# Kernel tuning notes

Measured on AMD Instinct MI355X. Metric: run time of the kernel, lower is better.

Reference implementation:

```python
import jax, jax.numpy as jnp
import numpy as np

D = 4096          # input_dims
P = 1             # p in Get_Atten_map_mc
NUM_IMG = 16
N_PER = 64        # objects per image
R_PER = 512       # relations per image
LN_EPS = 1e-5


def _linear_params(key, out_dim, in_dim):
    kw, kb = jax.random.split(key)
    w = jax.random.normal(kw, (out_dim, in_dim), jnp.float32) * 0.02
    b = jax.random.normal(kb, (out_dim,), jnp.float32) * 0.02
    return w, b


def setup_inputs() -> dict:
    key = jax.random.key(0)
    ks = jax.random.split(key, 12)
    N = NUM_IMG * N_PER
    R = NUM_IMG * R_PER

    obj_feats = jax.random.normal(ks[0], (N, D), jnp.float32)
    phr_feats = jax.random.normal(ks[1], (R, D), jnp.float32)

    # im_inds: uniform N_PER objects per image
    im_inds = jnp.repeat(jnp.arange(NUM_IMG, dtype=jnp.int64), N_PER)

    # rel_inds: [img_idx, subj_global, obj_global], R_PER rels per image,
    # subject/object indices local-to-image then offset to global ids.
    subj_loc = jax.random.randint(ks[2], (NUM_IMG, R_PER), 0, N_PER)
    obj_loc = jax.random.randint(ks[3], (NUM_IMG, R_PER), 0, N_PER)
    offs = (jnp.arange(NUM_IMG) * N_PER)[:, None]
    img_col = jnp.repeat(jnp.arange(NUM_IMG), R_PER)
    rel_inds = jnp.stack(
        [img_col, (subj_loc + offs).reshape(-1), (obj_loc + offs).reshape(-1)], axis=1
    ).astype(jnp.int64)

    Ws_w, Ws_b = _linear_params(ks[4], D, D)       # ws
    Wo_w, Wo_b = _linear_params(ks[5], D, D)       # wo
    Ww_w, Ww_b = _linear_params(ks[6], P, D)       # w (attention logits)
    Wc_w, Wc_b = _linear_params(ks[7], D // 2, D)  # conv Linear
    Wt1_w, Wt1_b = _linear_params(ks[8], D // 4, D)
    Wt2_w, Wt2_b = _linear_params(ks[9], D, D // 4)
    ln_g = jnp.ones((D // 4,), jnp.float32)
    ln_b = jnp.zeros((D // 4,), jnp.float32)

    return {
        "obj_feats": obj_feats, "phr_feats": phr_feats,
        "im_inds": im_inds, "rel_inds": rel_inds, "num_img": NUM_IMG,
        "Ws_w": Ws_w, "Ws_b": Ws_b, "Wo_w": Wo_w, "Wo_b": Wo_b,
        "Ww_w": Ww_w, "Ww_b": Ww_b, "Wc_w": Wc_w, "Wc_b": Wc_b,
        "Wt1_w": Wt1_w, "Wt1_b": Wt1_b, "ln_g": ln_g, "ln_b": ln_b,
        "Wt2_w": Wt2_w, "Wt2_b": Wt2_b,
    }


def reference(obj_feats, phr_feats, im_inds, rel_inds, num_img,
              Ws_w, Ws_b, Wo_w, Wo_b, Ww_w, Ww_b, Wc_w, Wc_b,
              Wt1_w, Wt1_b, ln_g, ln_b, Wt2_w, Wt2_b):
    N, d = obj_feats.shape
    n_per = N // num_img
    R = rel_inds.shape[0]
    r_per = R // num_img
    p = Ww_w.shape[0]

    # ws/wo projections over all objects (original recomputes them per image
    # on the full obj_feats -- identical math, computed once here).
    ws_all = obj_feats @ Ws_w.T + Ws_b
    wo_all = obj_feats @ Wo_w.T + Wo_b

    subj = rel_inds[:, 1]
    objc = rel_inds[:, 2]
    prod = ws_all[subj] * wo_all[objc]               # [R, D]
    atten_f = (prod * phr_feats) @ Ww_w.T + Ww_b     # [R, p]

    # conv on object features
    conv_all = jax.nn.relu(obj_feats @ Wc_w.T + Wc_b)  # [N, D/2]

    subj_i = subj.reshape(num_img, r_per)
    objc_i = objc.reshape(num_img, r_per)
    af_i = atten_f.reshape(num_img, r_per, p)
    conv_i = conv_all.reshape(num_img, n_per, -1)

    self_mask = 1.0 - jnp.eye(n_per, dtype=jnp.float32)[:, :, None]  # [n,n,1]

    def per_image(s, o, af, conv_feats):
        head = jnp.minimum(s.min(), o.min())
        A = jnp.zeros((n_per, n_per, p), jnp.float32).at[s - head, o - head].add(af)
        A = jax.nn.sigmoid(A) * self_mask
        A = A / A.sum(1)                               # [n,n,p] / [n,p] (col-normalize)
        A2 = jnp.concatenate([A, A.transpose(1, 0, 2)], axis=-1)  # [n,n,2p]
        # mc_matmul: concat of per-channel mm -> channel-major reshape
        return jnp.einsum('ijc,jd->icd', A2, conv_feats).reshape(n_per, -1)

    ctx = jax.vmap(per_image)(subj_i, objc_i, af_i, conv_i)  # [num_img, n, 2p*D/2]
    ctx = ctx.reshape(N, -1)                                  # [N, D]

    # trans: Linear -> LayerNorm -> ReLU -> Linear
    h = ctx @ Wt1_w.T + Wt1_b
    mu = h.mean(-1, keepdims=True)
    var = ((h - mu) ** 2).mean(-1, keepdims=True)
    h = (h - mu) * jax.lax.rsqrt(var + LN_EPS) * ln_g + ln_b
    h = jax.nn.relu(h)
    out = h @ Wt2_w.T + Wt2_b

    return jax.nn.relu(obj_feats + out)
```

## Files before the change

### kernel.cpp

```cpp
#include <hip/hip_runtime.h>
#include <hip/hip_bf16.h>
#include <math.h>

#define D_   4096
#define NIMG 16
#define NPER 64
#define RPER 512
#define NTOT 1024
#define RTOT 8192
#define DC   2048
#define DT   1024
#define LDO  10240

typedef __attribute__((ext_vector_type(4))) float f32x4;
typedef __attribute__((ext_vector_type(8))) short bf16x8;

#define GLD16(gp, lp) __builtin_amdgcn_global_load_lds( \
    (const __attribute__((address_space(1))) unsigned int*)(gp), \
    (__attribute__((address_space(3))) unsigned int*)(lp), 16, 0, 0)

struct Cast4 {
    const float* src0; const float* src1; const float* src2; const float* src3;
    __hip_bfloat16* dst0; __hip_bfloat16* dst1; __hip_bfloat16* dst2; __hip_bfloat16* dst3;
    int s1, s2, s3;
};

__global__ __launch_bounds__(256) void cast_multi(Cast4 a)
{
    const int b = blockIdx.x;
    const float* s; __hip_bfloat16* d; int rb;
    if (b < a.s1)      { s = a.src0; d = a.dst0; rb = b; }
    else if (b < a.s2) { s = a.src1; d = a.dst1; rb = b - a.s1; }
    else if (b < a.s3) { s = a.src2; d = a.dst2; rb = b - a.s2; }
    else               { s = a.src3; d = a.dst3; rb = b - a.s3; }
    const int i = (rb * 256 + threadIdx.x) * 8;
    float4 v0 = *(const float4*)(s + i);
    float4 v1 = *(const float4*)(s + i + 4);
    union { __hip_bfloat16 h[8]; ushort4 u[2]; } cv;
    cv.h[0] = __float2bfloat16(v0.x); cv.h[1] = __float2bfloat16(v0.y);
    cv.h[2] = __float2bfloat16(v0.z); cv.h[3] = __float2bfloat16(v0.w);
    cv.h[4] = __float2bfloat16(v1.x); cv.h[5] = __float2bfloat16(v1.y);
    cv.h[6] = __float2bfloat16(v1.z); cv.h[7] = __float2bfloat16(v1.w);
    *(ushort4*)(d + i)     = cv.u[0];
    *(ushort4*)(d + i + 4) = cv.u[1];
}

__global__ __launch_bounds__(256) void concat_bias(
    const float* __restrict__ b0, const float* __restrict__ b1,
    const float* __restrict__ b2, float* __restrict__ cb)
{
    const int i = blockIdx.x * 256 + threadIdx.x;
    float v;
    if (i < 4096) v = b0[i];
    else if (i < 8192) v = b1[i - 4096];
    else v = b2[i - 8192];
    cb[i] = v;
}

template<int BM, int BN>
__global__ __launch_bounds__(256) void gemm_p2(
    const ushort* __restrict__ A, const ushort* __restrict__ B,
    const float* __restrict__ bias, const float* __restrict__ resid,
    float* __restrict__ C, int M, int K, int ldc, int mode, int reluStart)
{
    constexpr int MREP = BM / 32;
    constexpr int NREP = BN / 32;
    constexpr int SLOTS = (BM + BN) * 4;
    constexpr int NPW = SLOTS / 256;
    constexpr int BUFE = SLOTS * 8;

    __shared__ ushort lds[3][BUFE];

    const int t = threadIdx.x;
    const int lane = t & 63;
    const int wid = t >> 6;
    const int wr = wid >> 1, wc = wid & 1;

    const int MT = M / BM;
    const int G = gridDim.x;
    const int bid = blockIdx.x;
    const int wgid = (bid & 7) * (G >> 3) + (bid >> 3);
    const int nt = wgid / MT, mt = wgid % MT;
    const int bm = mt * BM, bn = nt * BN;

    const ushort* gp[NPW];
    int loff[NPW];
#pragma unroll
    for (int i = 0; i < NPW; ++i) {
        const int slot = i * 256 + t;
        const bool isA = slot < BM * 4;
        const int s2 = isA ? slot : slot - BM * 4;
        const int row = s2 >> 2;
        const int q = (s2 & 3) ^ (row & 3);
        gp[i] = (isA ? A + (size_t)(bm + row) * K : B + (size_t)(bn + row) * K) + q * 8;
        loff[i] = slot * 8;
    }

    auto stage = [&](int b, int kpos) {
#pragma unroll
        for (int i = 0; i < NPW; ++i) GLD16(gp[i] + kpos, &lds[b][loff[i]]);
    };

    int aoff[MREP], boff[NREP];
    const int sx = (((lane >> 4) ^ (lane & 3))) << 3;
#pragma unroll
    for (int m = 0; m < MREP; ++m)
        aoff[m] = (wr * (BM / 2) + (lane & 15) + m * 16) * 32 + sx;
#pragma unroll
    for (int n = 0; n < NREP; ++n)
        boff[n] = BM * 32 + (wc * (BN / 2) + (lane & 15) + n * 16) * 32 + sx;

    f32x4 acc[MREP][NREP] = {};

    const int NT = K >> 5;
    stage(0, 0);
    stage(1, 32);
    if constexpr (NPW == 2) asm volatile("s_waitcnt vmcnt(2)" ::: "memory");
    else if constexpr (NPW == 3) asm volatile("s_waitcnt vmcnt(3)" ::: "memory");
    else asm volatile("s_waitcnt vmcnt(4)" ::: "memory");
    __builtin_amdgcn_sched_barrier(0);
    __builtin_amdgcn_s_barrier();
    __builtin_amdgcn_sched_barrier(0);

    for (int tt = 0; tt < NT; ++tt) {
        const bool pf = (tt + 2 < NT);
        if (pf) stage((tt + 2) % 3, (tt + 2) << 5);
        __builtin_amdgcn_sched_barrier(0);

        const ushort* lb = lds[tt % 3];
        bf16x8 af[MREP], bfv[NREP];
#pragma unroll
        for (int m = 0; m < MREP; ++m) af[m] = *(const bf16x8*)(lb + aoff[m]);
#pragma unroll
        for (int n = 0; n < NREP; ++n) bfv[n] = *(const bf16x8*)(lb + boff[n]);
#pragma unroll
        for (int m = 0; m < MREP; ++m)
#pragma unroll
            for (int n = 0; n < NREP; ++n)
                acc[m][n] = __builtin_amdgcn_mfma_f32_16x16x32_bf16(
                    af[m], bfv[n], acc[m][n], 0, 0, 0);

        __builtin_amdgcn_sched_barrier(0);
        if (pf) {
            if constexpr (NPW == 2) asm volatile("s_waitcnt vmcnt(2)" ::: "memory");
            else if constexpr (NPW == 3) asm volatile("s_waitcnt vmcnt(3)" ::: "memory");
            else asm volatile("s_waitcnt vmcnt(4)" ::: "memory");
        } else {
            asm volatile("s_waitcnt vmcnt(0)" ::: "memory");
        }
        __builtin_amdgcn_sched_barrier(0);
        __builtin_amdgcn_s_barrier();
        __builtin_amdgcn_sched_barrier(0);
    }

    const int col0 = bn + wc * (BN / 2) + (lane & 15);
    const int row0 = bm + wr * (BM / 2) + ((lane >> 4) << 2);
#pragma unroll
    for (int m = 0; m < MREP; ++m) {
#pragma unroll
        for (int n = 0; n < NREP; ++n) {
            const int cn = col0 + n * 16;
            const float bz = bias[cn];
#pragma unroll
            for (int rg = 0; rg < 4; ++rg) {
                const int gm = row0 + m * 16 + rg;
                float v = acc[m][n][rg] + bz;
                if (mode == 2) v = fmaxf(v + resid[(size_t)gm * ldc + cn], 0.f);
                else if (mode == 3 && cn >= reluStart) v = fmaxf(v, 0.f);
                C[(size_t)gm * ldc + cn] = v;
            }
        }
    }
}

__global__ __launch_bounds__(256) void atten_kernel(
    const float* __restrict__ allout, const float* __restrict__ phr,
    const int* __restrict__ rel, const float* __restrict__ Www,
    const float* __restrict__ Wwb, float* __restrict__ atten)
{
    const int r = blockIdx.x;
    const int s = rel[r * 3 + 1], o = rel[r * 3 + 2];
    const int t = threadIdx.x;
    const float4* pws = (const float4*)(allout + (size_t)s * LDO);
    const float4* pwo = (const float4*)(allout + (size_t)o * LDO + 4096);
    const float4* pph = (const float4*)(phr + (size_t)r * D_);
    const float4* pww = (const float4*)Www;
    float sum = 0.f;
    for (int qq = t; qq < D_ / 4; qq += 256) {
        float4 a = pws[qq], b = pwo[qq], c = pph[qq], w = pww[qq];
        sum += a.x * b.x * c.x * w.x + a.y * b.y * c.y * w.y
             + a.z * b.z * c.z * w.z + a.w * b.w * c.w * w.w;
    }
    for (int off = 32; off > 0; off >>= 1) sum += __shfl_down(sum, off);
    __shared__ float red[4];
    if ((t & 63) == 0) red[t >> 6] = sum;
    __syncthreads();
    if (t == 0) atten[r] = red[0] + red[1] + red[2] + red[3] + Wwb[0];
}

__global__ __launch_bounds__(256) void build_A(
    const int* __restrict__ rel, const float* __restrict__ atten,
    float* __restrict__ Anorm)
{
    const int g = blockIdx.x;
    const int t = threadIdx.x;
    __shared__ float Am[64][64];
    __shared__ float S[64];
    __shared__ int headSh;
    for (int i = t; i < 4096; i += 256) ((float*)Am)[i] = 0.f;
    if (t == 0) headSh = 0x7fffffff;

    int lmin = 0x7fffffff;
    for (int rr = t; rr < RPER; rr += 256) {
        const int base = (g * RPER + rr) * 3;
        lmin = min(lmin, min(rel[base + 1], rel[base + 2]));
    }
    for (int off = 32; off > 0; off >>= 1) lmin = min(lmin, __shfl_down(lmin, off));
    __syncthreads();
    if ((t & 63) == 0) atomicMin(&headSh, lmin);
    __syncthreads();
    const int head = headSh;

    for (int rr = t; rr < RPER; rr += 256) {
        const int base = (g * RPER + rr) * 3;
        atomicAdd(&Am[rel[base + 1] - head][rel[base + 2] - head],
                  atten[g * RPER + rr]);
    }
    __syncthreads();

    for (int idx = t; idx < 4096; idx += 256) {
        const int i = idx >> 6, j = idx & 63;
        float v = 1.f / (1.f + expf(-Am[i][j]));
        if (i == j) v = 0.f;
        Am[i][j] = v;
    }
    __syncthreads();

    if (t < 64) {
        float sum = 0.f;
        for (int k = 0; k < 64; ++k) sum += Am[t][k];
        S[t] = sum;
    }
    __syncthreads();

    float* outg = Anorm + (size_t)g * 4096;
    for (int idx = t; idx < 4096; idx += 256) {
        const int j = idx & 63;
        outg[idx] = ((const float*)Am)[idx] / S[j];
    }
}

__device__ __forceinline__ void fma4(float4& d, float s, const float4 c) {
    d.x = fmaf(s, c.x, d.x); d.y = fmaf(s, c.y, d.y);
    d.z = fmaf(s, c.z, d.z); d.w = fmaf(s, c.w, d.w);
}
__device__ __forceinline__ void st4bf(__hip_bfloat16* p, float4 v) {
    union { __hip_bfloat16 h[4]; ushort4 u; } cv;
    cv.h[0] = __float2bfloat16(v.x); cv.h[1] = __float2bfloat16(v.y);
    cv.h[2] = __float2bfloat16(v.z); cv.h[3] = __float2bfloat16(v.w);
    *(ushort4*)p = cv.u;
}

__global__ __launch_bounds__(256) void ctx_kernel(
    const float* __restrict__ Anorm, const float* __restrict__ allout,
    __hip_bfloat16* __restrict__ ctx)
{
    const int g = blockIdx.x >> 6;
    const int i = blockIdx.x & 63;
    const int t = threadIdx.x;
    __shared__ float Arow[64], Acol[64];
    if (t < 64) Arow[t] = Anorm[(size_t)g * 4096 + i * 64 + t];
    else if (t < 128) { const int j = t - 64; Acol[j] = Anorm[(size_t)g * 4096 + j * 64 + i]; }
    __syncthreads();

    const float* cg = allout + (size_t)g * NPER * LDO + 8192;
    float4 a0 = {0,0,0,0}, a1 = a0, a2 = a0, a3 = a0;
    for (int j = 0; j < 64; ++j) {
        const float ar = Arow[j], ac = Acol[j];
        float4 c0 = *(const float4*)(cg + (size_t)j * LDO + (t << 2));
        float4 c1 = *(const float4*)(cg + (size_t)j * LDO + 1024 + (t << 2));
        fma4(a0, ar, c0); fma4(a1, ar, c1);
        fma4(a2, ac, c0); fma4(a3, ac, c1);
    }
    __hip_bfloat16* crow = ctx + (size_t)(g * NPER + i) * D_;
    st4bf(crow + (t << 2),        a0);
    st4bf(crow + 1024 + (t << 2), a1);
    st4bf(crow + 2048 + (t << 2), a2);
    st4bf(crow + 3072 + (t << 2), a3);
}

__global__ __launch_bounds__(256) void ln_relu_kernel(
    const float* __restrict__ h, const float* __restrict__ gamma,
    const float* __restrict__ beta, __hip_bfloat16* __restrict__ hb)
{
    const int row = blockIdx.x;
    const int t = threadIdx.x;
    const float* hr = h + (size_t)row * DT;
    float4 v = *(const float4*)(hr + (t << 2));
    float s  = v.x + v.y + v.z + v.w;
    float ss = v.x * v.x + v.y * v.y + v.z * v.z + v.w * v.w;
    for (int off = 32; off > 0; off >>= 1) {
        s  += __shfl_down(s, off);
        ss += __shfl_down(ss, off);
    }
    __shared__ float rs[4], rss[4];
    if ((t & 63) == 0) { rs[t >> 6] = s; rss[t >> 6] = ss; }
    __syncthreads();
    const float tot  = rs[0] + rs[1] + rs[2] + rs[3];
    const float tot2 = rss[0] + rss[1] + rss[2] + rss[3];
    const float mu   = tot * (1.f / DT);
    const float var  = tot2 * (1.f / DT) - mu * mu;
    const float rstd = rsqrtf(var + 1e-5f);
    float4 g4 = *(const float4*)(gamma + (t << 2));
    float4 b4 = *(const float4*)(beta + (t << 2));
    float4 o;
    o.x = fmaxf(fmaf((v.x - mu) * rstd, g4.x, b4.x), 0.f);
    o.y = fmaxf(fmaf((v.y - mu) * rstd, g4.y, b4.y), 0.f);
    o.z = fmaxf(fmaf((v.z - mu) * rstd, g4.z, b4.z), 0.f);
    o.w = fmaxf(fmaf((v.w - mu) * rstd, g4.w, b4.w), 0.f);
    st4bf(hb + (size_t)row * DT + (t << 2), o);
}

extern "C" void kernel_launch(void* const* d_in, const int* in_sizes, int n_in,
                              void* d_out, int out_size, void* d_ws, size_t ws_size,
                              hipStream_t stream)
{
    const float* obj   = (const float*)d_in[0];
    const float* phr   = (const float*)d_in[1];
    const int*   rel   = (const int*)d_in[3];
    const float* Ws_w  = (const float*)d_in[5];
    const float* Ws_b  = (const float*)d_in[6];
    const float* Wo_w  = (const float*)d_in[7];
    const float* Wo_b  = (const float*)d_in[8];
    const float* Ww_w  = (const float*)d_in[9];
    const float* Ww_b  = (const float*)d_in[10];
    const float* Wc_w  = (const float*)d_in[11];
    const float* Wc_b  = (const float*)d_in[12];
    const float* Wt1_w = (const float*)d_in[13];
    const float* Wt1_b = (const float*)d_in[14];
    const float* ln_g  = (const float*)d_in[15];
    const float* ln_b  = (const float*)d_in[16];
    const float* Wt2_w = (const float*)d_in[17];
    const float* Wt2_b = (const float*)d_in[18];
    float* out = (float*)d_out;

    float* ws = (float*)d_ws;
    __hip_bfloat16* wbuf   = (__hip_bfloat16*)ws;
    __hip_bfloat16* wbuf_t1 = wbuf;
    __hip_bfloat16* wbuf_t2 = wbuf + 4194304;
    __hip_bfloat16* obj_bf = (__hip_bfloat16*)(ws + 20971520);
    __hip_bfloat16* ctx_bf = obj_bf;
    float* allout = ws + 23068672;
    float* h_f32  = allout;
    __hip_bfloat16* h_bf = (__hip_bfloat16*)(allout + 1048576);
    float* atten  = ws + 33554432;
    float* Anorm  = ws + 33562624;
    float* cbias  = ws + 33628160;

    const dim3 blk(256);

    Cast4 c1;
    c1.src0 = obj;  c1.dst0 = obj_bf;
    c1.src1 = Ws_w; c1.dst1 = wbuf;
    c1.src2 = Wo_w; c1.dst2 = wbuf + 16777216;
    c1.src3 = Wc_w; c1.dst3 = wbuf + 33554432;
    c1.s1 = 2048; c1.s2 = 10240; c1.s3 = 18432;
    cast_multi<<<dim3(22528), blk, 0, stream>>>(c1);

    concat_bias<<<dim3(40), blk, 0, stream>>>(Ws_b, Wo_b, Wc_b, cbias);

    gemm_p2<128, 128><<<dim3(640), blk, 0, stream>>>(
        (const ushort*)obj_bf, (const ushort*)wbuf, cbias, nullptr,
        allout, NTOT, D_, LDO, 3, 8192);

    Cast4 c2;
    c2.src0 = Wt1_w; c2.dst0 = wbuf_t1;
    c2.src1 = Wt2_w; c2.dst1 = wbuf_t2;
    c2.src2 = Wt1_w; c2.dst2 = wbuf_t1;
    c2.src3 = Wt1_w; c2.dst3 = wbuf_t1;
    c2.s1 = 2048; c2.s2 = 1 << 30; c2.s3 = 1 << 30;
    cast_multi<<<dim3(4096), blk, 0, stream>>>(c2);

    atten_kernel<<<dim3(RTOT), blk, 0, stream>>>(allout, phr, rel, Ww_w, Ww_b, atten);
    build_A<<<dim3(NIMG), blk, 0, stream>>>(rel, atten, Anorm);
    ctx_kernel<<<dim3(1024), blk, 0, stream>>>(Anorm, allout, ctx_bf);

    gemm_p2<64, 64><<<dim3(256), blk, 0, stream>>>(
        (const ushort*)ctx_bf, (const ushort*)wbuf_t1, Wt1_b, nullptr,
        h_f32, NTOT, D_, DT, 0, 0);
    ln_relu_kernel<<<dim3(NTOT), blk, 0, stream>>>(h_f32, ln_g, ln_b, h_bf);
    gemm_p2<128, 128><<<dim3(256), blk, 0, stream>>>(
        (const ushort*)h_bf, (const ushort*)wbuf_t2, Wt2_b, obj,
        out, NTOT, DT, D_, 2, 0);
}
```

Baseline: 326.7 us.

## Fuse fp32-to-bf16 weight conversion into GEMM B-operand loading

Removes the separate cast kernels that converted all weight matrices (about 40M fp32 elements) to bf16 in workspace. The GEMMs now read fp32 weights directly into registers, convert them, and write bf16 into LDS, while the activation operand keeps the async global-to-LDS path. The object cast and bias concatenation are merged into one launch. This avoids a large write-then-read round trip, but the GEMMs now load twice the weight bytes and spend VALU and register time converting inside the main loop.

```diff
diff --git a/kernel.cpp b/kernel.cpp
--- a/kernel.cpp
+++ b/kernel.cpp
@@ -19,55 +19,53 @@
     (const __attribute__((address_space(1))) unsigned int*)(gp), \
     (__attribute__((address_space(3))) unsigned int*)(lp), 16, 0, 0)
 
-struct Cast4 {
-    const float* src0; const float* src1; const float* src2; const float* src3;
-    __hip_bfloat16* dst0; __hip_bfloat16* dst1; __hip_bfloat16* dst2; __hip_bfloat16* dst3;
-    int s1, s2, s3;
-};
-
-__global__ __launch_bounds__(256) void cast_multi(Cast4 a)
-{
-    const int b = blockIdx.x;
-    const float* s; __hip_bfloat16* d; int rb;
-    if (b < a.s1)      { s = a.src0; d = a.dst0; rb = b; }
-    else if (b < a.s2) { s = a.src1; d = a.dst1; rb = b - a.s1; }
-    else if (b < a.s3) { s = a.src2; d = a.dst2; rb = b - a.s2; }
-    else               { s = a.src3; d = a.dst3; rb = b - a.s3; }
-    const int i = (rb * 256 + threadIdx.x) * 8;
-    float4 v0 = *(const float4*)(s + i);
-    float4 v1 = *(const float4*)(s + i + 4);
-    union { __hip_bfloat16 h[8]; ushort4 u[2]; } cv;
-    cv.h[0] = __float2bfloat16(v0.x); cv.h[1] = __float2bfloat16(v0.y);
-    cv.h[2] = __float2bfloat16(v0.z); cv.h[3] = __float2bfloat16(v0.w);
-    cv.h[4] = __float2bfloat16(v1.x); cv.h[5] = __float2bfloat16(v1.y);
-    cv.h[6] = __float2bfloat16(v1.z); cv.h[7] = __float2bfloat16(v1.w);
-    *(ushort4*)(d + i)     = cv.u[0];
-    *(ushort4*)(d + i + 4) = cv.u[1];
-}
-
-__global__ __launch_bounds__(256) void concat_bias(
+template<int N> __device__ __forceinline__ void waitvm() {
+    asm volatile("s_waitcnt vmcnt(%0)" :: "n"(N) : "memory");
+}
+
+__global__ __launch_bounds__(256) void cast_obj_bias(
+    const float* __restrict__ obj, __hip_bfloat16* __restrict__ obj_bf,
     const float* __restrict__ b0, const float* __restrict__ b1,
     const float* __restrict__ b2, float* __restrict__ cb)
 {
-    const int i = blockIdx.x * 256 + threadIdx.x;
-    float v;
-    if (i < 4096) v = b0[i];
-    else if (i < 8192) v = b1[i - 4096];
-    else v = b2[i - 8192];
-    cb[i] = v;
+    const int b = blockIdx.x;
+    if (b < 2048) {
+        const int i = (b * 256 + threadIdx.x) * 8;
+        float4 v0 = *(const float4*)(obj + i);
+        float4 v1 = *(const float4*)(obj + i + 4);
+        union { __hip_bfloat16 h[8]; ushort4 u[2]; } cv;
+        cv.h[0] = __float2bfloat16(v0.x); cv.h[1] = __float2bfloat16(v0.y);
+        cv.h[2] = __float2bfloat16(v0.z); cv.h[3] = __float2bfloat16(v0.w);
+        cv.h[4] = __float2bfloat16(v1.x); cv.h[5] = __float2bfloat16(v1.y);
+        cv.h[6] = __float2bfloat16(v1.z); cv.h[7] = __float2bfloat16(v1.w);
+        *(ushort4*)(obj_bf + i)     = cv.u[0];
+        *(ushort4*)(obj_bf + i + 4) = cv.u[1];
+    } else {
+        const int i = (b - 2048) * 256 + threadIdx.x;
+        float v;
+        if (i < 4096) v = b0[i];
+        else if (i < 8192) v = b1[i - 4096];
+        else v = b2[i - 8192];
+        cb[i] = v;
+    }
 }
 
 template<int BM, int BN>
-__global__ __launch_bounds__(256) void gemm_p2(
-    const ushort* __restrict__ A, const ushort* __restrict__ B,
+__global__ __launch_bounds__(256) void gemm_h(
+    const ushort* __restrict__ A,
+    const float* __restrict__ B0, const float* __restrict__ B1,
+    const float* __restrict__ B2, int ns1, int ns2,
     const float* __restrict__ bias, const float* __restrict__ resid,
     float* __restrict__ C, int M, int K, int ldc, int mode, int reluStart)
 {
     constexpr int MREP = BM / 32;
     constexpr int NREP = BN / 32;
-    constexpr int SLOTS = (BM + BN) * 4;
-    constexpr int NPW = SLOTS / 256;
-    constexpr int BUFE = SLOTS * 8;
+    constexpr int SA = BM * 4;
+    constexpr int SB = BN * 4;
+    constexpr int NA = SA / 256;
+    constexpr int NB = SB / 256;
+    constexpr int INFLIGHT = NA + 2 * NB;
+    constexpr int BUFE = (SA + SB) * 8;
 
     __shared__ ushort lds[3][BUFE];
 
@@ -83,22 +81,53 @@
     const int nt = wgid / MT, mt = wgid % MT;
     const int bm = mt * BM, bn = nt * BN;
 
-    const ushort* gp[NPW];
-    int loff[NPW];
-#pragma unroll
-    for (int i = 0; i < NPW; ++i) {
+    const ushort* gpa[NA];
+    int lofa[NA];
+#pragma unroll
+    for (int i = 0; i < NA; ++i) {
         const int slot = i * 256 + t;
-        const bool isA = slot < BM * 4;
-        const int s2 = isA ? slot : slot - BM * 4;
-        const int row = s2 >> 2;
-        const int q = (s2 & 3) ^ (row & 3);
-        gp[i] = (isA ? A + (size_t)(bm + row) * K : B + (size_t)(bn + row) * K) + q * 8;
-        loff[i] = slot * 8;
-    }
-
-    auto stage = [&](int b, int kpos) {
-#pragma unroll
-        for (int i = 0; i < NPW; ++i) GLD16(gp[i] + kpos, &lds[b][loff[i]]);
+        const int row = slot >> 2;
+        const int q = (slot & 3) ^ (row & 3);
+        gpa[i] = A + (size_t)(bm + row) * K + q * 8;
+        lofa[i] = slot * 8;
+    }
+    const float* gpb[NB];
+    int lofb[NB];
+#pragma unroll
+    for (int i = 0; i < NB; ++i) {
+        const int sb = i * 256 + t;
+        const int row = sb >> 2;
+        const int q = (sb & 3) ^ (row & 3);
+        const int gn = bn + row;
+        const float* bp = (gn < ns1) ? B0 + (size_t)gn * K
+                        : (gn < ns2) ? B1 + (size_t)(gn - ns1) * K
+                                     : B2 + (size_t)(gn - ns2) * K;
+        gpb[i] = bp + q * 8;
+        lofb[i] = (SA + sb) * 8;
+    }
+
+    auto stageA = [&](int b, int kpos) {
+#pragma unroll
+        for (int i = 0; i < NA; ++i) GLD16(gpa[i] + kpos, &lds[b][lofa[i]]);
+    };
+    auto loadB = [&](f32x4 (&br)[NB][2], int kpos) {
+#pragma unroll
+        for (int i = 0; i < NB; ++i) {
+            br[i][0] = *(const f32x4*)(gpb[i] + kpos);
+            br[i][1] = *(const f32x4*)(gpb[i] + kpos + 4);
+        }
+    };
+    auto writeB = [&](f32x4 (&br)[NB][2], int b) {
+#pragma unroll
+        for (int i = 0; i < NB; ++i) {
+            union { __hip_bfloat16 h[8]; uint4 q; } cv;
+#pragma unroll
+            for (int j = 0; j < 4; ++j) {
+                cv.h[j]     = __float2bfloat16(br[i][0][j]);
+                cv.h[4 + j] = __float2bfloat16(br[i][1][j]);
+            }
+            *(uint4*)&lds[b][lofb[i]] = cv.q;
+        }
     };
 
     int aoff[MREP], boff[NREP];
@@ -108,23 +137,28 @@
         aoff[m] = (wr * (BM / 2) + (lane & 15) + m * 16) * 32 + sx;
 #pragma unroll
     for (int n = 0; n < NREP; ++n)
-        boff[n] = BM * 32 + (wc * (BN / 2) + (lane & 15) + n * 16) * 32 + sx;
+        boff[n] = SA * 8 + (wc * (BN / 2) + (lane & 15) + n * 16) * 32 + sx;
 
     f32x4 acc[MREP][NREP] = {};
+    f32x4 br0[NB][2], br1[NB][2];
 
     const int NT = K >> 5;
-    stage(0, 0);
-    stage(1, 32);
-    if constexpr (NPW == 2) asm volatile("s_waitcnt vmcnt(2)" ::: "memory");
-    else if constexpr (NPW == 3) asm volatile("s_waitcnt vmcnt(3)" ::: "memory");
-    else asm volatile("s_waitcnt vmcnt(4)" ::: "memory");
+
+    stageA(0, 0);  loadB(br0, 0);
+    stageA(1, 32); loadB(br1, 32);
+    waitvm<INFLIGHT>();
+    writeB(br0, 0);
+    asm volatile("s_waitcnt lgkmcnt(0)" ::: "memory");
     __builtin_amdgcn_sched_barrier(0);
     __builtin_amdgcn_s_barrier();
     __builtin_amdgcn_sched_barrier(0);
 
-    for (int tt = 0; tt < NT; ++tt) {
-        const bool pf = (tt + 2 < NT);
-        if (pf) stage((tt + 2) % 3, (tt + 2) << 5);
+    auto step = [&](int tt, auto& brW, auto& brL) {
+        const bool more = (tt + 2 < NT);
+        if (more) {
+            stageA((tt + 2) % 3, (tt + 2) << 5);
+            loadB(brL, (tt + 2) << 5);
+        }
         __builtin_amdgcn_sched_barrier(0);
 
         const ushort* lb = lds[tt % 3];
@@ -139,18 +173,22 @@
             for (int n = 0; n < NREP; ++n)
                 acc[m][n] = __builtin_amdgcn_mfma_f32_16x16x32_bf16(
                     af[m], bfv[n], acc[m][n], 0, 0, 0);
-
         __builtin_amdgcn_sched_barrier(0);
-        if (pf) {
-            if constexpr (NPW == 2) asm volatile("s_waitcnt vmcnt(2)" ::: "memory");
-            else if constexpr (NPW == 3) asm volatile("s_waitcnt vmcnt(3)" ::: "memory");
-            else asm volatile("s_waitcnt vmcnt(4)" ::: "memory");
-        } else {
-            asm volatile("s_waitcnt vmcnt(0)" ::: "memory");
+
+        if (tt + 1 < NT) {
+            if (more) waitvm<INFLIGHT>(); else waitvm<0>();
+            __builtin_amdgcn_sched_barrier(0);
+            writeB(brW, (tt + 1) % 3);
+            asm volatile("s_waitcnt lgkmcnt(0)" ::: "memory");
+            __builtin_amdgcn_sched_barrier(0);
+            __builtin_amdgcn_s_barrier();
+            __builtin_amdgcn_sched_barrier(0);
         }
-        __builtin_amdgcn_sched_barrier(0);
-        __builtin_amdgcn_s_barrier();
-        __builtin_amdgcn_sched_barrier(0);
+    };
+
+    for (int tt = 0; tt < NT; tt += 2) {
+        step(tt,     br1, br0);
+        step(tt + 1, br0, br1);
     }
 
     const int col0 = bn + wc * (BN / 2) + (lane & 15);
@@ -345,51 +383,33 @@
     float* out = (float*)d_out;
 
     float* ws = (float*)d_ws;
-    __hip_bfloat16* wbuf   = (__hip_bfloat16*)ws;
-    __hip_bfloat16* wbuf_t1 = wbuf;
-    __hip_bfloat16* wbuf_t2 = wbuf + 4194304;
-    __hip_bfloat16* obj_bf = (__hip_bfloat16*)(ws + 20971520);
+    __hip_bfloat16* obj_bf = (__hip_bfloat16*)ws;
     __hip_bfloat16* ctx_bf = obj_bf;
-    float* allout = ws + 23068672;
+    float* allout = ws + 2097152;
     float* h_f32  = allout;
     __hip_bfloat16* h_bf = (__hip_bfloat16*)(allout + 1048576);
-    float* atten  = ws + 33554432;
-    float* Anorm  = ws + 33562624;
-    float* cbias  = ws + 33628160;
+    float* atten  = ws + 12582912;
+    float* Anorm  = ws + 12591104;
+    float* cbias  = ws + 12656640;
 
     const dim3 blk(256);
-
-    Cast4 c1;
-    c1.src0 = obj;  c1.dst0 = obj_bf;
-    c1.src1 = Ws_w; c1.dst1 = wbuf;
-    c1.src2 = Wo_w; c1.dst2 = wbuf + 16777216;
-    c1.src3 = Wc_w; c1.dst3 = wbuf + 33554432;
-    c1.s1 = 2048; c1.s2 = 10240; c1.s3 = 18432;
-    cast_multi<<<dim3(22528), blk, 0, stream>>>(c1);
-
-    concat_bias<<<dim3(40), blk, 0, stream>>>(Ws_b, Wo_b, Wc_b, cbias);
-
-    gemm_p2<128, 128><<<dim3(640), blk, 0, stream>>>(
-        (const ushort*)obj_bf, (const ushort*)wbuf, cbias, nullptr,
-        allout, NTOT, D_, LDO, 3, 8192);
-
-    Cast4 c2;
-    c2.src0 = Wt1_w; c2.dst0 = wbuf_t1;
-    c2.src1 = Wt2_w; c2.dst1 = wbuf_t2;
-    c2.src2 = Wt1_w; c2.dst2 = wbuf_t1;
-    c2.src3 = Wt1_w; c2.dst3 = wbuf_t1;
-    c2.s1 = 2048; c2.s2 = 1 << 30; c2.s3 = 1 << 30;
-    cast_multi<<<dim3(4096), blk, 0, stream>>>(c2);
+    const int BIG = 1 << 30;
+
+    cast_obj_bias<<<dim3(2088), blk, 0, stream>>>(obj, obj_bf, Ws_b, Wo_b, Wc_b, cbias);
+
+    gemm_h<128, 128><<<dim3(640), blk, 0, stream>>>(
+        (const ushort*)obj_bf, Ws_w, Wo_w, Wc_w, 4096, 8192,
+        cbias, nullptr, allout, NTOT, D_, LDO, 3, 8192);
 
     atten_kernel<<<dim3(RTOT), blk, 0, stream>>>(allout, phr, rel, Ww_w, Ww_b, atten);
     build_A<<<dim3(NIMG), blk, 0, stream>>>(rel, atten, Anorm);
     ctx_kernel<<<dim3(1024), blk, 0, stream>>>(Anorm, allout, ctx_bf);
 
-    gemm_p2<64, 64><<<dim3(256), blk, 0, stream>>>(
-        (const ushort*)ctx_bf, (const ushort*)wbuf_t1, Wt1_b, nullptr,
-        h_f32, NTOT, D_, DT, 0, 0);
+    gemm_h<64, 64><<<dim3(256), blk, 0, stream>>>(
+        (const ushort*)ctx_bf, Wt1_w, Wt1_w, Wt1_w, BIG, BIG,
+        Wt1_b, nullptr, h_f32, NTOT, D_, DT, 0, 0);
     ln_relu_kernel<<<dim3(NTOT), blk, 0, stream>>>(h_f32, ln_g, ln_b, h_bf);
-    gemm_p2<128, 128><<<dim3(256), blk, 0, stream>>>(
-        (const ushort*)h_bf, (const ushort*)wbuf_t2, Wt2_b, obj,
-        out, NTOT, DT, D_, 2, 0);
-}
+    gemm_h<128, 128><<<dim3(256), blk, 0, stream>>>(
+        (const ushort*)h_bf, Wt2_w, Wt2_w, Wt2_w, BIG, BIG,
+        Wt2_b, obj, out, NTOT, DT, D_, 2, 0);
+}
```

Result: slower. 494.1 us (+51.2%).

## Reassociate attention mixing after Wt1 projection and fuse mixing with LayerNorm

Applied to the files above, without the earlier changes.

The code now computes the first trans projection on the conv features (conv @ Wt1 split into subject and object halves) before applying the per-image attention matrix, rather than building the 4096-wide context and multiplying it by Wt1. The Wt1 weight is rearranged during casting so a single GEMM with K=2048 produces both halves, and the A-mixing, bias add, LayerNorm and ReLU are fused into one kernel. The first GEMM writes the conv output straight to bf16 with ReLU, and the row stride shrinks to 8192. Casting and bias concatenation are merged into one launch, and the LDS swizzle pattern is changed. This removes the ctx buffer, the wide K=4096 GEMM and a separate LN pass, at the cost of a different rounding order.

```diff
diff --git a/kernel.cpp b/kernel.cpp
--- a/kernel.cpp
+++ b/kernel.cpp
@@ -10,7 +10,7 @@
 #define RTOT 8192
 #define DC   2048
 #define DT   1024
-#define LDO  10240
+#define LDA  8192
 
 typedef __attribute__((ext_vector_type(4))) float f32x4;
 typedef __attribute__((ext_vector_type(8))) short bf16x8;
@@ -19,49 +19,88 @@
     (const __attribute__((address_space(1))) unsigned int*)(gp), \
     (__attribute__((address_space(3))) unsigned int*)(lp), 16, 0, 0)
 
-struct Cast4 {
-    const float* src0; const float* src1; const float* src2; const float* src3;
-    __hip_bfloat16* dst0; __hip_bfloat16* dst1; __hip_bfloat16* dst2; __hip_bfloat16* dst3;
-    int s1, s2, s3;
-};
-
-__global__ __launch_bounds__(256) void cast_multi(Cast4 a)
+template<int N> __device__ __forceinline__ void waitvm() {
+    asm volatile("s_waitcnt vmcnt(%0)" :: "n"(N) : "memory");
+}
+
+__device__ __forceinline__ void fma4(float4& d, float s, const float4 c) {
+    d.x = fmaf(s, c.x, d.x); d.y = fmaf(s, c.y, d.y);
+    d.z = fmaf(s, c.z, d.z); d.w = fmaf(s, c.w, d.w);
+}
+__device__ __forceinline__ void st4bf(__hip_bfloat16* p, float4 v) {
+    union { __hip_bfloat16 h[4]; ushort4 u; } cv;
+    cv.h[0] = __float2bfloat16(v.x); cv.h[1] = __float2bfloat16(v.y);
+    cv.h[2] = __float2bfloat16(v.z); cv.h[3] = __float2bfloat16(v.w);
+    *(ushort4*)p = cv.u;
+}
+
+__global__ __launch_bounds__(256) void cast_all(
+    const float* __restrict__ obj, __hip_bfloat16* __restrict__ obj_bf,
+    const float* __restrict__ Ws, const float* __restrict__ Wo,
+    const float* __restrict__ Wc, __hip_bfloat16* __restrict__ wbuf,
+    const float* __restrict__ b0, const float* __restrict__ b1,
+    const float* __restrict__ b2, float* __restrict__ cb)
 {
     const int b = blockIdx.x;
-    const float* s; __hip_bfloat16* d; int rb;
-    if (b < a.s1)      { s = a.src0; d = a.dst0; rb = b; }
-    else if (b < a.s2) { s = a.src1; d = a.dst1; rb = b - a.s1; }
-    else if (b < a.s3) { s = a.src2; d = a.dst2; rb = b - a.s2; }
-    else               { s = a.src3; d = a.dst3; rb = b - a.s3; }
-    const int i = (rb * 256 + threadIdx.x) * 8;
-    float4 v0 = *(const float4*)(s + i);
-    float4 v1 = *(const float4*)(s + i + 4);
+    if (b < 22528) {
+        const float* s; __hip_bfloat16* d; int rb;
+        if (b < 2048)       { s = obj; d = obj_bf;          rb = b; }
+        else if (b < 10240) { s = Ws;  d = wbuf;            rb = b - 2048; }
+        else if (b < 18432) { s = Wo;  d = wbuf + 16777216; rb = b - 10240; }
+        else                { s = Wc;  d = wbuf + 33554432; rb = b - 18432; }
+        const int i = (rb * 256 + threadIdx.x) * 8;
+        float4 v0 = *(const float4*)(s + i);
+        float4 v1 = *(const float4*)(s + i + 4);
+        union { __hip_bfloat16 h[8]; ushort4 u[2]; } cv;
+        cv.h[0] = __float2bfloat16(v0.x); cv.h[1] = __float2bfloat16(v0.y);
+        cv.h[2] = __float2bfloat16(v0.z); cv.h[3] = __float2bfloat16(v0.w);
+        cv.h[4] = __float2bfloat16(v1.x); cv.h[5] = __float2bfloat16(v1.y);
+        cv.h[6] = __float2bfloat16(v1.z); cv.h[7] = __float2bfloat16(v1.w);
+        *(ushort4*)(d + i)     = cv.u[0];
+        *(ushort4*)(d + i + 4) = cv.u[1];
+    } else {
+        const int i = (b - 22528) * 256 + threadIdx.x;
+        float v;
+        if (i < 4096) v = b0[i];
+        else if (i < 8192) v = b1[i - 4096];
+        else v = b2[i - 8192];
+        cb[i] = v;
+    }
+}
+
+__global__ __launch_bounds__(256) void cast2(
+    const float* __restrict__ Wt1, const float* __restrict__ Wt2,
+    __hip_bfloat16* __restrict__ wt1r, __hip_bfloat16* __restrict__ wt2b)
+{
+    const int b = blockIdx.x;
+    const int t = threadIdx.x;
+    const float* s; __hip_bfloat16* d;
+    if (b < 2048) {
+        const int r = b, c = t * 8;
+        s = Wt1 + (size_t)(r & 1023) * 4096 + (r >> 10) * 2048 + c;
+        d = wt1r + (size_t)r * 2048 + c;
+    } else {
+        const int i = ((b - 2048) * 256 + t) * 8;
+        s = Wt2 + i;
+        d = wt2b + i;
+    }
+    float4 v0 = *(const float4*)s;
+    float4 v1 = *(const float4*)(s + 4);
     union { __hip_bfloat16 h[8]; ushort4 u[2]; } cv;
     cv.h[0] = __float2bfloat16(v0.x); cv.h[1] = __float2bfloat16(v0.y);
     cv.h[2] = __float2bfloat16(v0.z); cv.h[3] = __float2bfloat16(v0.w);
     cv.h[4] = __float2bfloat16(v1.x); cv.h[5] = __float2bfloat16(v1.y);
     cv.h[6] = __float2bfloat16(v1.z); cv.h[7] = __float2bfloat16(v1.w);
-    *(ushort4*)(d + i)     = cv.u[0];
-    *(ushort4*)(d + i + 4) = cv.u[1];
-}
-
-__global__ __launch_bounds__(256) void concat_bias(
-    const float* __restrict__ b0, const float* __restrict__ b1,
-    const float* __restrict__ b2, float* __restrict__ cb)
-{
-    const int i = blockIdx.x * 256 + threadIdx.x;
-    float v;
-    if (i < 4096) v = b0[i];
-    else if (i < 8192) v = b1[i - 4096];
-    else v = b2[i - 8192];
-    cb[i] = v;
+    *(ushort4*)d       = cv.u[0];
+    *(ushort4*)(d + 4) = cv.u[1];
 }
 
 template<int BM, int BN>
 __global__ __launch_bounds__(256) void gemm_p2(
     const ushort* __restrict__ A, const ushort* __restrict__ B,
     const float* __restrict__ bias, const float* __restrict__ resid,
-    float* __restrict__ C, int M, int K, int ldc, int mode, int reluStart)
+    float* __restrict__ C, __hip_bfloat16* __restrict__ C2,
+    int M, int K, int ldc, int mode, int reluStart)
 {
     constexpr int MREP = BM / 32;
     constexpr int NREP = BN / 32;
@@ -91,7 +130,7 @@
         const bool isA = slot < BM * 4;
         const int s2 = isA ? slot : slot - BM * 4;
         const int row = s2 >> 2;
-        const int q = (s2 & 3) ^ (row & 3);
+        const int q = (s2 & 3) ^ ((row >> 1) & 3);
         gp[i] = (isA ? A + (size_t)(bm + row) * K : B + (size_t)(bn + row) * K) + q * 8;
         loff[i] = slot * 8;
     }
@@ -102,7 +141,7 @@
     };
 
     int aoff[MREP], boff[NREP];
-    const int sx = (((lane >> 4) ^ (lane & 3))) << 3;
+    const int sx = (((lane >> 4) ^ ((lane >> 1) & 3))) << 3;
 #pragma unroll
     for (int m = 0; m < MREP; ++m)
         aoff[m] = (wr * (BM / 2) + (lane & 15) + m * 16) * 32 + sx;
@@ -115,9 +154,9 @@
     const int NT = K >> 5;
     stage(0, 0);
     stage(1, 32);
-    if constexpr (NPW == 2) asm volatile("s_waitcnt vmcnt(2)" ::: "memory");
-    else if constexpr (NPW == 3) asm volatile("s_waitcnt vmcnt(3)" ::: "memory");
-    else asm volatile("s_waitcnt vmcnt(4)" ::: "memory");
+    if constexpr (NPW == 2) waitvm<2>();
+    else if constexpr (NPW == 3) waitvm<3>();
+    else waitvm<4>();
     __builtin_amdgcn_sched_barrier(0);
     __builtin_amdgcn_s_barrier();
     __builtin_amdgcn_sched_barrier(0);
@@ -142,11 +181,11 @@
 
         __builtin_amdgcn_sched_barrier(0);
         if (pf) {
-            if constexpr (NPW == 2) asm volatile("s_waitcnt vmcnt(2)" ::: "memory");
-            else if constexpr (NPW == 3) asm volatile("s_waitcnt vmcnt(3)" ::: "memory");
-            else asm volatile("s_waitcnt vmcnt(4)" ::: "memory");
+            if constexpr (NPW == 2) waitvm<2>();
+            else if constexpr (NPW == 3) waitvm<3>();
+            else waitvm<4>();
         } else {
-            asm volatile("s_waitcnt vmcnt(0)" ::: "memory");
+            waitvm<0>();
         }
         __builtin_amdgcn_sched_barrier(0);
         __builtin_amdgcn_s_barrier();
@@ -160,14 +199,24 @@
 #pragma unroll
         for (int n = 0; n < NREP; ++n) {
             const int cn = col0 + n * 16;
-            const float bz = bias[cn];
+            const float bz = bias ? bias[cn] : 0.f;
 #pragma unroll
             for (int rg = 0; rg < 4; ++rg) {
                 const int gm = row0 + m * 16 + rg;
                 float v = acc[m][n][rg] + bz;
-                if (mode == 2) v = fmaxf(v + resid[(size_t)gm * ldc + cn], 0.f);
-                else if (mode == 3 && cn >= reluStart) v = fmaxf(v, 0.f);
-                C[(size_t)gm * ldc + cn] = v;
+                if (mode == 2) {
+                    v = fmaxf(v + resid[(size_t)gm * ldc + cn], 0.f);
+                    C[(size_t)gm * ldc + cn] = v;
+                } else if (mode == 4) {
+                    if (cn < reluStart) {
+                        C[(size_t)gm * ldc + cn] = v;
+                    } else {
+                        C2[(size_t)gm * 2048 + (cn - 8192)] =
+                            __float2bfloat16(fmaxf(v, 0.f));
+                    }
+                } else {
+                    C[(size_t)gm * ldc + cn] = v;
+                }
             }
         }
     }
@@ -181,8 +230,8 @@
     const int r = blockIdx.x;
     const int s = rel[r * 3 + 1], o = rel[r * 3 + 2];
     const int t = threadIdx.x;
-    const float4* pws = (const float4*)(allout + (size_t)s * LDO);
-    const float4* pwo = (const float4*)(allout + (size_t)o * LDO + 4096);
+    const float4* pws = (const float4*)(allout + (size_t)s * LDA);
+    const float4* pwo = (const float4*)(allout + (size_t)o * LDA + 4096);
     const float4* pph = (const float4*)(phr + (size_t)r * D_);
     const float4* pww = (const float4*)Www;
     float sum = 0.f;
@@ -250,53 +299,30 @@
     }
 }
 
-__device__ __forceinline__ void fma4(float4& d, float s, const float4 c) {
-    d.x = fmaf(s, c.x, d.x); d.y = fmaf(s, c.y, d.y);
-    d.z = fmaf(s, c.z, d.z); d.w = fmaf(s, c.w, d.w);
-}
-__device__ __forceinline__ void st4bf(__hip_bfloat16* p, float4 v) {
-    union { __hip_bfloat16 h[4]; ushort4 u; } cv;
-    cv.h[0] = __float2bfloat16(v.x); cv.h[1] = __float2bfloat16(v.y);
-    cv.h[2] = __float2bfloat16(v.z); cv.h[3] = __float2bfloat16(v.w);
-    *(ushort4*)p = cv.u;
-}
-
-__global__ __launch_bounds__(256) void ctx_kernel(
-    const float* __restrict__ Anorm, const float* __restrict__ allout,
-    __hip_bfloat16* __restrict__ ctx)
+__global__ __launch_bounds__(256) void amult_ln(
+    const float* __restrict__ Anorm, const float* __restrict__ P,
+    const float* __restrict__ w1b, const float* __restrict__ gamma,
+    const float* __restrict__ beta, __hip_bfloat16* __restrict__ hb)
 {
     const int g = blockIdx.x >> 6;
     const int i = blockIdx.x & 63;
     const int t = threadIdx.x;
-    __shared__ float Arow[64], Acol[64];
-    if (t < 64) Arow[t] = Anorm[(size_t)g * 4096 + i * 64 + t];
-    else if (t < 128) { const int j = t - 64; Acol[j] = Anorm[(size_t)g * 4096 + j * 64 + i]; }
-    __syncthreads();
-
-    const float* cg = allout + (size_t)g * NPER * LDO + 8192;
-    float4 a0 = {0,0,0,0}, a1 = a0, a2 = a0, a3 = a0;
+    __shared__ float Ar[64], Ac[64];
+    if (t < 64) Ar[t] = Anorm[(size_t)g * 4096 + i * 64 + t];
+    else if (t < 128) { const int j = t - 64; Ac[j] = Anorm[(size_t)g * 4096 + j * 64 + i]; }
+    __syncthreads();
+
+    const float* pg = P + (size_t)g * 64 * 2048;
+    float4 v = {0, 0, 0, 0};
     for (int j = 0; j < 64; ++j) {
-        const float ar = Arow[j], ac = Acol[j];
-        float4 c0 = *(const float4*)(cg + (size_t)j * LDO + (t << 2));
-        float4 c1 = *(const float4*)(cg + (size_t)j * LDO + 1024 + (t << 2));
-        fma4(a0, ar, c0); fma4(a1, ar, c1);
-        fma4(a2, ac, c0); fma4(a3, ac, c1);
-    }
-    __hip_bfloat16* crow = ctx + (size_t)(g * NPER + i) * D_;
-    st4bf(crow + (t << 2),        a0);
-    st4bf(crow + 1024 + (t << 2), a1);
-    st4bf(crow + 2048 + (t << 2), a2);
-    st4bf(crow + 3072 + (t << 2), a3);
-}
-
-__global__ __launch_bounds__(256) void ln_relu_kernel(
-    const float* __restrict__ h, const float* __restrict__ gamma,
-    const float* __restrict__ beta, __hip_bfloat16* __restrict__ hb)
-{
-    const int row = blockIdx.x;
-    const int t = threadIdx.x;
-    const float* hr = h + (size_t)row * DT;
-    float4 v = *(const float4*)(hr + (t << 2));
+        float4 p1 = *(const float4*)(pg + (size_t)j * 2048 + (t << 2));
+        float4 p2 = *(const float4*)(pg + (size_t)j * 2048 + 1024 + (t << 2));
+        fma4(v, Ar[j], p1);
+        fma4(v, Ac[j], p2);
+    }
+    float4 b0 = *(const float4*)(w1b + (t << 2));
+    v.x += b0.x; v.y += b0.y; v.z += b0.z; v.w += b0.w;
+
     float s  = v.x + v.y + v.z + v.w;
     float ss = v.x * v.x + v.y * v.y + v.z * v.z + v.w * v.w;
     for (int off = 32; off > 0; off >>= 1) {
@@ -318,7 +344,7 @@
     o.y = fmaxf(fmaf((v.y - mu) * rstd, g4.y, b4.y), 0.f);
     o.z = fmaxf(fmaf((v.z - mu) * rstd, g4.z, b4.z), 0.f);
     o.w = fmaxf(fmaf((v.w - mu) * rstd, g4.w, b4.w), 0.f);
-    st4bf(hb + (size_t)row * DT + (t << 2), o);
+    st4bf(hb + (size_t)(g * 64 + i) * DT + (t << 2), o);
 }
 
 extern "C" void kernel_launch(void* const* d_in, const int* in_sizes, int n_in,
@@ -346,50 +372,38 @@
 
     float* ws = (float*)d_ws;
     __hip_bfloat16* wbuf   = (__hip_bfloat16*)ws;
-    __hip_bfloat16* wbuf_t1 = wbuf;
-    __hip_bfloat16* wbuf_t2 = wbuf + 4194304;
+    __hip_bfloat16* wt1r   = (__hip_bfloat16*)ws;
+    __hip_bfloat16* wt2b   = (__hip_bfloat16*)(ws + 2097152);
     __hip_bfloat16* obj_bf = (__hip_bfloat16*)(ws + 20971520);
-    __hip_bfloat16* ctx_bf = obj_bf;
     float* allout = ws + 23068672;
-    float* h_f32  = allout;
-    __hip_bfloat16* h_bf = (__hip_bfloat16*)(allout + 1048576);
-    float* atten  = ws + 33554432;
-    float* Anorm  = ws + 33562624;
-    float* cbias  = ws + 33628160;
+    float* Pbuf   = allout;
+    __hip_bfloat16* h_bf = (__hip_bfloat16*)(allout + 2097152);
+    __hip_bfloat16* conv_bf = (__hip_bfloat16*)(ws + 31457280);
+    float* atten  = ws + 32505856;
+    float* Anorm  = ws + 32514048;
+    float* cbias  = ws + 32579584;
 
     const dim3 blk(256);
 
-    Cast4 c1;
-    c1.src0 = obj;  c1.dst0 = obj_bf;
-    c1.src1 = Ws_w; c1.dst1 = wbuf;
-    c1.src2 = Wo_w; c1.dst2 = wbuf + 16777216;
-    c1.src3 = Wc_w; c1.dst3 = wbuf + 33554432;
-    c1.s1 = 2048; c1.s2 = 10240; c1.s3 = 18432;
-    cast_multi<<<dim3(22528), blk, 0, stream>>>(c1);
-
-    concat_bias<<<dim3(40), blk, 0, stream>>>(Ws_b, Wo_b, Wc_b, cbias);
+    cast_all<<<dim3(22568), blk, 0, stream>>>(
+        obj, obj_bf, Ws_w, Wo_w, Wc_w, wbuf, Ws_b, Wo_b, Wc_b, cbias);
 
     gemm_p2<128, 128><<<dim3(640), blk, 0, stream>>>(
         (const ushort*)obj_bf, (const ushort*)wbuf, cbias, nullptr,
-        allout, NTOT, D_, LDO, 3, 8192);
-
-    Cast4 c2;
-    c2.src0 = Wt1_w; c2.dst0 = wbuf_t1;
-    c2.src1 = Wt2_w; c2.dst1 = wbuf_t2;
-    c2.src2 = Wt1_w; c2.dst2 = wbuf_t1;
-    c2.src3 = Wt1_w; c2.dst3 = wbuf_t1;
-    c2.s1 = 2048; c2.s2 = 1 << 30; c2.s3 = 1 << 30;
-    cast_multi<<<dim3(4096), blk, 0, stream>>>(c2);
+        allout, conv_bf, NTOT, D_, LDA, 4, 8192);
+
+    cast2<<<dim3(4096), blk, 0, stream>>>(Wt1_w, Wt2_w, wt1r, wt2b);
 
     atten_kernel<<<dim3(RTOT), blk, 0, stream>>>(allout, phr, rel, Ww_w, Ww_b, atten);
     build_A<<<dim3(NIMG), blk, 0, stream>>>(rel, atten, Anorm);
-    ctx_kernel<<<dim3(1024), blk, 0, stream>>>(Anorm, allout, ctx_bf);
-
-    gemm_p2<64, 64><<<dim3(256), blk, 0, stream>>>(
-        (const ushort*)ctx_bf, (const ushort*)wbuf_t1, Wt1_b, nullptr,
-        h_f32, NTOT, D_, DT, 0, 0);
-    ln_relu_kernel<<<dim3(NTOT), blk, 0, stream>>>(h_f32, ln_g, ln_b, h_bf);
+
+    gemm_p2<64, 64><<<dim3(512), blk, 0, stream>>>(
+        (const ushort*)conv_bf, (const ushort*)wt1r, nullptr, nullptr,
+        Pbuf, nullptr, NTOT, DC, DC, 0, 0);
+
+    amult_ln<<<dim3(1024), blk, 0, stream>>>(Anorm, Pbuf, Wt1_b, ln_g, ln_b, h_bf);
+
     gemm_p2<128, 128><<<dim3(256), blk, 0, stream>>>(
-        (const ushort*)h_bf, (const ushort*)wbuf_t2, Wt2_b, obj,
-        out, NTOT, DT, D_, 2, 0);
-}
+        (const ushort*)h_bf, (const ushort*)wt2b, Wt2_b, obj,
+        out, nullptr, NTOT, DT, D_, 2, 0);
+}
```

After: 318.0 us. 1.03x faster.
